# Optimization experiments

Hardware: AMD Instinct MI355X
Metric: run time of the kernel (lower is better)

Reference implementation:

```python
import jax, jax.numpy as jnp
import numpy as np

NUM_HEAD = 32
NUM_KV_HEAD = 8
HEAD_DIM = 128
EMBED_DIM = 4096
GROUP = NUM_HEAD // NUM_KV_HEAD + 2  # 6: 4 q slots + 1 k + 1 v
TOKENS = 64


def setup_inputs() -> dict:
    key = jax.random.key(0)
    k1, k2, k3 = jax.random.split(key, 3)
    inp = jax.random.normal(k1, (TOKENS, EMBED_DIM), dtype=jnp.float32)
    # fused GQA weight layout from load_parameter: [embed_dim, num_kv_head, group, head_dim]
    weight = jax.random.normal(k2, (EMBED_DIM, NUM_KV_HEAD, GROUP, HEAD_DIM), dtype=jnp.float32) * 0.02
    bias = jax.random.normal(k3, (NUM_KV_HEAD, GROUP, HEAD_DIM), dtype=jnp.float32) * 0.02
    return {"input": inp, "weight": weight, "bias": bias}


def reference(input, weight, bias):
    # fused grouped QKV GEMM (mm_qkv_group_out):
    # out[t, kv, g, d] = sum_e input[t, e] * weight[e, kv, g, d] + bias[kv, g, d]
    out = jnp.einsum('te,ekgd->tkgd', input, weight) + bias
    T = input.shape[0]
    q = out[:, :, : GROUP - 2, :].reshape(T, NUM_HEAD * HEAD_DIM)
    k = out[:, :, GROUP - 2, :].reshape(T, NUM_KV_HEAD * HEAD_DIM)
    v = out[:, :, GROUP - 1, :].reshape(T, NUM_KV_HEAD * HEAD_DIM)
    return (q, k, v)
```

## Files before the change

kernel.cpp:

```cpp
#include <hip/hip_runtime.h>


#define N_COLS 6144
#define K_DIM  4096
#define Q_SZ   (64 * 4096)
#define K_OFF  Q_SZ
#define V_OFF  (Q_SZ + 64 * 1024)
#define OUT_ELEMS 393216
#define IN_ELEMS  262144

typedef __bf16 bf16x8 __attribute__((ext_vector_type(8)));
typedef float  f32x4  __attribute__((ext_vector_type(4)));
typedef unsigned short us8 __attribute__((ext_vector_type(8)));

__device__ unsigned short g_abuf[IN_ELEMS];

__device__ __forceinline__ unsigned short f2bf_rne(float f) {
    unsigned int u = __float_as_uint(f);
    u += 0x7FFFu + ((u >> 16) & 1u);
    return (unsigned short)(u >> 16);
}

__device__ __forceinline__ int out_index(int t, int n) {
    const int kv = n / 768;
    const int g  = (n >> 7) % 6;
    const int d  = n & 127;
    if (g < 4)  return t * 4096 + kv * 512 + g * 128 + d;
    if (g == 4) return K_OFF + t * 1024 + kv * 128 + d;
    return V_OFF + t * 1024 + kv * 128 + d;
}

__global__ __launch_bounds__(256)
void init_kernel(const float* __restrict__ in, const float* __restrict__ bias,
                 float* __restrict__ out) {
    const int i = blockIdx.x * 256 + threadIdx.x;
    if (i < IN_ELEMS) g_abuf[i] = f2bf_rne(in[i]);
    if (i < OUT_ELEMS) {
        const int d   = i & 127;
        const int g   = (i >> 7) % 6;
        const int kvt = i / 768;
        const int kv  = kvt & 7;
        const int t   = kvt >> 3;
        out[out_index(t, kv * 768 + g * 128 + d)] = bias[(kv * 6 + g) * 128 + d];
    }
}

__global__ __launch_bounds__(256, 3)
void qkv_gemm(const float* __restrict__ w, float* __restrict__ out) {
    __shared__ float red[4][64][17];

    const int tid  = threadIdx.x;
    const int nt   = blockIdx.x >> 1;
    const int kh   = blockIdx.x & 1;
    const int n0   = nt * 16;
    const int wid  = tid >> 6;
    const int lane = tid & 63;
    const int l15  = lane & 15;
    const int kblk = lane >> 4;
    const int ks   = kh * 2048 + wid * 512;

    f32x4 acc[4] = {{0.f,0.f,0.f,0.f},{0.f,0.f,0.f,0.f},
                    {0.f,0.f,0.f,0.f},{0.f,0.f,0.f,0.f}};

    const float* bbase = w + (size_t)(ks + kblk * 8) * N_COLS + n0 + l15;
    const unsigned short* abase = g_abuf + l15 * K_DIM + ks + kblk * 8;

    #pragma unroll 4
    for (int kk = 0; kk < 512; kk += 32) {
        const float* bp = bbase + (size_t)kk * N_COLS;
        unsigned int b[8];
        #pragma unroll
        for (int j = 0; j < 8; ++j)
            b[j] = __float_as_uint(bp[(size_t)j * N_COLS]);

        us8 au0 = *(const us8*)(abase + kk);
        us8 au1 = *(const us8*)(abase + 16 * K_DIM + kk);
        us8 au2 = *(const us8*)(abase + 32 * K_DIM + kk);
        us8 au3 = *(const us8*)(abase + 48 * K_DIM + kk);

        union { unsigned int u[4]; us8 v; } pk;
        #pragma unroll
        for (int j = 0; j < 4; ++j) {
            const unsigned int lo = b[2 * j]     + 0x8000u;
            const unsigned int hi = b[2 * j + 1] + 0x8000u;
            pk.u[j] = (hi & 0xFFFF0000u) | (lo >> 16);
        }
        const bf16x8 bf = __builtin_bit_cast(bf16x8, pk.v);

        acc[0] = __builtin_amdgcn_mfma_f32_16x16x32_bf16(
                     __builtin_bit_cast(bf16x8, au0), bf, acc[0], 0, 0, 0);
        acc[1] = __builtin_amdgcn_mfma_f32_16x16x32_bf16(
                     __builtin_bit_cast(bf16x8, au1), bf, acc[1], 0, 0, 0);
        acc[2] = __builtin_amdgcn_mfma_f32_16x16x32_bf16(
                     __builtin_bit_cast(bf16x8, au2), bf, acc[2], 0, 0, 0);
        acc[3] = __builtin_amdgcn_mfma_f32_16x16x32_bf16(
                     __builtin_bit_cast(bf16x8, au3), bf, acc[3], 0, 0, 0);
    }

    #pragma unroll
    for (int tc = 0; tc < 4; ++tc)
        #pragma unroll
        for (int r = 0; r < 4; ++r)
            red[wid][lane][tc * 4 + r] = acc[tc][r];
    __syncthreads();

    const int l  = tid & 63;
    const int i0 = (tid >> 6) * 4;
    const int rl15  = l & 15;
    const int rkblk = l >> 4;
    #pragma unroll
    for (int r2 = 0; r2 < 4; ++r2) {
        const int i = i0 + r2;
        const float s = red[0][l][i] + red[1][l][i] + red[2][l][i] + red[3][l][i];
        const int tc = i >> 2, r = i & 3;
        const int t = tc * 16 + rkblk * 4 + r;
        atomicAdd(&out[out_index(t, n0 + rl15)], s);
    }
}

extern "C" void kernel_launch(void* const* d_in, const int* in_sizes, int n_in,
                              void* d_out, int out_size, void* d_ws, size_t ws_size,
                              hipStream_t stream) {
    const float* in   = (const float*)d_in[0];
    const float* w    = (const float*)d_in[1];
    const float* bias = (const float*)d_in[2];
    float* out = (float*)d_out;

    init_kernel<<<(OUT_ELEMS + 255) / 256, 256, 0, stream>>>(in, bias, out);
    qkv_gemm<<<768, 256, 0, stream>>>(w, out);
}
```

Before: 187.8 us.

## Split K four ways and software-pipeline weight loads with register double buffering

Raises the K split from two to four so the grid launches twice as many blocks, each warp covering 256 K elements instead of 512. The inner loop is fully unrolled and register double-buffered, prefetching the next slice of weights and activations before issuing MFMAs on the current one. Launch bounds ask for five blocks per CU to increase occupancy. The aim is more memory-level parallelism while streaming the 100MB fp32 weight, at the cost of twice as many atomic adds into the output.

Result: no change. 189.6 us (+0.9%).

```diff
diff --git a/kernel.cpp b/kernel.cpp
--- a/kernel.cpp
+++ b/kernel.cpp
@@ -8,10 +8,14 @@
 #define V_OFF  (Q_SZ + 64 * 1024)
 #define OUT_ELEMS 393216
 #define IN_ELEMS  262144
+#define KSPLIT 4
+#define KW     256
+#define NIT    (KW / 32)
 
 typedef __bf16 bf16x8 __attribute__((ext_vector_type(8)));
 typedef float  f32x4  __attribute__((ext_vector_type(4)));
 typedef unsigned short us8 __attribute__((ext_vector_type(8)));
+typedef unsigned int   u32x4 __attribute__((ext_vector_type(4)));
 
 __device__ unsigned short g_abuf[IN_ELEMS];
 
@@ -45,19 +49,30 @@
     }
 }
 
-__global__ __launch_bounds__(256, 3)
+__device__ __forceinline__ bf16x8 pack_bf16(const float* b) {
+    u32x4 pk;
+    #pragma unroll
+    for (int j = 0; j < 4; ++j) {
+        const unsigned int lo = __float_as_uint(b[2 * j])     + 0x8000u;
+        const unsigned int hi = __float_as_uint(b[2 * j + 1]) + 0x8000u;
+        pk[j] = (hi & 0xFFFF0000u) | (lo >> 16);
+    }
+    return __builtin_bit_cast(bf16x8, pk);
+}
+
+__global__ __launch_bounds__(256, 5)
 void qkv_gemm(const float* __restrict__ w, float* __restrict__ out) {
     __shared__ float red[4][64][17];
 
     const int tid  = threadIdx.x;
-    const int nt   = blockIdx.x >> 1;
-    const int kh   = blockIdx.x & 1;
+    const int nt   = blockIdx.x >> 2;
+    const int kq   = blockIdx.x & 3;
     const int n0   = nt * 16;
     const int wid  = tid >> 6;
     const int lane = tid & 63;
     const int l15  = lane & 15;
     const int kblk = lane >> 4;
-    const int ks   = kh * 2048 + wid * 512;
+    const int ks   = kq * 1024 + wid * KW;
 
     f32x4 acc[4] = {{0.f,0.f,0.f,0.f},{0.f,0.f,0.f,0.f},
                     {0.f,0.f,0.f,0.f},{0.f,0.f,0.f,0.f}};
@@ -65,36 +80,42 @@
     const float* bbase = w + (size_t)(ks + kblk * 8) * N_COLS + n0 + l15;
     const unsigned short* abase = g_abuf + l15 * K_DIM + ks + kblk * 8;
 
-    #pragma unroll 4
-    for (int kk = 0; kk < 512; kk += 32) {
-        const float* bp = bbase + (size_t)kk * N_COLS;
-        unsigned int b[8];
-        #pragma unroll
-        for (int j = 0; j < 8; ++j)
-            b[j] = __float_as_uint(bp[(size_t)j * N_COLS]);
+    float bc[8];
+    us8   ac[4];
+    #pragma unroll
+    for (int j = 0; j < 8; ++j) bc[j] = bbase[(size_t)j * N_COLS];
+    #pragma unroll
+    for (int t = 0; t < 4; ++t) ac[t] = *(const us8*)(abase + t * 16 * K_DIM);
 
-        us8 au0 = *(const us8*)(abase + kk);
-        us8 au1 = *(const us8*)(abase + 16 * K_DIM + kk);
-        us8 au2 = *(const us8*)(abase + 32 * K_DIM + kk);
-        us8 au3 = *(const us8*)(abase + 48 * K_DIM + kk);
+    #pragma unroll
+    for (int it = 0; it < NIT; ++it) {
+        float bn[8];
+        us8   an[4];
+        if (it + 1 < NIT) {
+            const float* bp = bbase + (size_t)(32 * (it + 1)) * N_COLS;
+            #pragma unroll
+            for (int j = 0; j < 8; ++j) bn[j] = bp[(size_t)j * N_COLS];
+            const unsigned short* ap = abase + 32 * (it + 1);
+            #pragma unroll
+            for (int t = 0; t < 4; ++t) an[t] = *(const us8*)(ap + t * 16 * K_DIM);
+        }
 
-        union { unsigned int u[4]; us8 v; } pk;
-        #pragma unroll
-        for (int j = 0; j < 4; ++j) {
-            const unsigned int lo = b[2 * j]     + 0x8000u;
-            const unsigned int hi = b[2 * j + 1] + 0x8000u;
-            pk.u[j] = (hi & 0xFFFF0000u) | (lo >> 16);
+        const bf16x8 bf = pack_bf16(bc);
+        acc[0] = __builtin_amdgcn_mfma_f32_16x16x32_bf16(
+                     __builtin_bit_cast(bf16x8, ac[0]), bf, acc[0], 0, 0, 0);
+        acc[1] = __builtin_amdgcn_mfma_f32_16x16x32_bf16(
+                     __builtin_bit_cast(bf16x8, ac[1]), bf, acc[1], 0, 0, 0);
+        acc[2] = __builtin_amdgcn_mfma_f32_16x16x32_bf16(
+                     __builtin_bit_cast(bf16x8, ac[2]), bf, acc[2], 0, 0, 0);
+        acc[3] = __builtin_amdgcn_mfma_f32_16x16x32_bf16(
+                     __builtin_bit_cast(bf16x8, ac[3]), bf, acc[3], 0, 0, 0);
+
+        if (it + 1 < NIT) {
+            #pragma unroll
+            for (int j = 0; j < 8; ++j) bc[j] = bn[j];
+            #pragma unroll
+            for (int t = 0; t < 4; ++t) ac[t] = an[t];
         }
-        const bf16x8 bf = __builtin_bit_cast(bf16x8, pk.v);
-
-        acc[0] = __builtin_amdgcn_mfma_f32_16x16x32_bf16(
-                     __builtin_bit_cast(bf16x8, au0), bf, acc[0], 0, 0, 0);
-        acc[1] = __builtin_amdgcn_mfma_f32_16x16x32_bf16(
-                     __builtin_bit_cast(bf16x8, au1), bf, acc[1], 0, 0, 0);
-        acc[2] = __builtin_amdgcn_mfma_f32_16x16x32_bf16(
-                     __builtin_bit_cast(bf16x8, au2), bf, acc[2], 0, 0, 0);
-        acc[3] = __builtin_amdgcn_mfma_f32_16x16x32_bf16(
-                     __builtin_bit_cast(bf16x8, au3), bf, acc[3], 0, 0, 0);
     }
 
     #pragma unroll
@@ -127,5 +148,5 @@
     float* out = (float*)d_out;
 
     init_kernel<<<(OUT_ELEMS + 255) / 256, 256, 0, stream>>>(in, bias, out);
-    qkv_gemm<<<768, 256, 0, stream>>>(w, out);
+    qkv_gemm<<<384 * KSPLIT, 256, 0, stream>>>(w, out);
 }
```

## Double-buffer global loads in QKV GEMM with inline asm and explicit vmcnt waits

Applied to the files above, without the earlier changes.

Replaces the compiler-scheduled K loop with a hand-written two-stage software pipeline. Weight and activation loads are issued through inline-asm global_load instructions into two register sets, and partial s_waitcnt vmcnt waits let one stage's MFMAs overlap the next stage's loads. Launch bounds are raised to 4 blocks per SIMD. The aim is to hide the latency of the memory-bound fp32 weight stream, at the cost of more live registers and fragile asm that assumes vmcnt ordering.

Result: no change. 186.5 us (-0.7%).

```diff
diff --git a/kernel.cpp b/kernel.cpp
--- a/kernel.cpp
+++ b/kernel.cpp
@@ -8,10 +8,13 @@
 #define V_OFF  (Q_SZ + 64 * 1024)
 #define OUT_ELEMS 393216
 #define IN_ELEMS  262144
+#define KSPLIT 2
+#define KW     512
+#define NIT    (KW / 32)
 
 typedef __bf16 bf16x8 __attribute__((ext_vector_type(8)));
 typedef float  f32x4  __attribute__((ext_vector_type(4)));
-typedef unsigned short us8 __attribute__((ext_vector_type(8)));
+typedef unsigned int u32x4 __attribute__((ext_vector_type(4)));
 
 __device__ unsigned short g_abuf[IN_ELEMS];
 
@@ -45,7 +48,56 @@
     }
 }
 
-__global__ __launch_bounds__(256, 3)
+__device__ __forceinline__ bf16x8 pack8(float f0, float f1, float f2, float f3,
+                                        float f4, float f5, float f6, float f7) {
+    u32x4 pk;
+    const float fs[8] = {f0, f1, f2, f3, f4, f5, f6, f7};
+    #pragma unroll
+    for (int j = 0; j < 4; ++j) {
+        const unsigned int lo = __float_as_uint(fs[2 * j])     + 0x8000u;
+        const unsigned int hi = __float_as_uint(fs[2 * j + 1]) + 0x8000u;
+        pk[j] = (hi & 0xFFFF0000u) | (lo >> 16);
+    }
+    return __builtin_bit_cast(bf16x8, pk);
+}
+
+#define ISSUE(P, kk) do {                                                     \
+    const float* _bp = bbase + (size_t)(kk) * N_COLS;                         \
+    asm volatile("global_load_dword %0, %1, off" : "=v"(P##_b0) : "v"(_bp + 0 * (size_t)N_COLS)); \
+    asm volatile("global_load_dword %0, %1, off" : "=v"(P##_b1) : "v"(_bp + 1 * (size_t)N_COLS)); \
+    asm volatile("global_load_dword %0, %1, off" : "=v"(P##_b2) : "v"(_bp + 2 * (size_t)N_COLS)); \
+    asm volatile("global_load_dword %0, %1, off" : "=v"(P##_b3) : "v"(_bp + 3 * (size_t)N_COLS)); \
+    asm volatile("global_load_dword %0, %1, off" : "=v"(P##_b4) : "v"(_bp + 4 * (size_t)N_COLS)); \
+    asm volatile("global_load_dword %0, %1, off" : "=v"(P##_b5) : "v"(_bp + 5 * (size_t)N_COLS)); \
+    asm volatile("global_load_dword %0, %1, off" : "=v"(P##_b6) : "v"(_bp + 6 * (size_t)N_COLS)); \
+    asm volatile("global_load_dword %0, %1, off" : "=v"(P##_b7) : "v"(_bp + 7 * (size_t)N_COLS)); \
+    const unsigned short* _ap = abase + (kk);                                 \
+    asm volatile("global_load_dwordx4 %0, %1, off" : "=v"(P##_a0) : "v"(_ap + 0 * 16 * K_DIM));   \
+    asm volatile("global_load_dwordx4 %0, %1, off" : "=v"(P##_a1) : "v"(_ap + 1 * 16 * K_DIM));   \
+    asm volatile("global_load_dwordx4 %0, %1, off" : "=v"(P##_a2) : "v"(_ap + 2 * 16 * K_DIM));   \
+    asm volatile("global_load_dwordx4 %0, %1, off" : "=v"(P##_a3) : "v"(_ap + 3 * 16 * K_DIM));   \
+} while (0)
+
+#define WAITB(P, cnt) \
+    asm volatile("s_waitcnt vmcnt(" #cnt ")"                                  \
+                 : "+v"(P##_b0), "+v"(P##_b1), "+v"(P##_b2), "+v"(P##_b3),    \
+                   "+v"(P##_b4), "+v"(P##_b5), "+v"(P##_b6), "+v"(P##_b7),    \
+                   "+v"(P##_a0), "+v"(P##_a1), "+v"(P##_a2), "+v"(P##_a3))
+
+#define CONSUME(P) do {                                                       \
+    const bf16x8 _bf = pack8(P##_b0, P##_b1, P##_b2, P##_b3,                  \
+                             P##_b4, P##_b5, P##_b6, P##_b7);                 \
+    acc[0] = __builtin_amdgcn_mfma_f32_16x16x32_bf16(                         \
+                 __builtin_bit_cast(bf16x8, P##_a0), _bf, acc[0], 0, 0, 0);   \
+    acc[1] = __builtin_amdgcn_mfma_f32_16x16x32_bf16(                         \
+                 __builtin_bit_cast(bf16x8, P##_a1), _bf, acc[1], 0, 0, 0);   \
+    acc[2] = __builtin_amdgcn_mfma_f32_16x16x32_bf16(                         \
+                 __builtin_bit_cast(bf16x8, P##_a2), _bf, acc[2], 0, 0, 0);   \
+    acc[3] = __builtin_amdgcn_mfma_f32_16x16x32_bf16(                         \
+                 __builtin_bit_cast(bf16x8, P##_a3), _bf, acc[3], 0, 0, 0);   \
+} while (0)
+
+__global__ __launch_bounds__(256, 4)
 void qkv_gemm(const float* __restrict__ w, float* __restrict__ out) {
     __shared__ float red[4][64][17];
 
@@ -57,7 +109,7 @@
     const int lane = tid & 63;
     const int l15  = lane & 15;
     const int kblk = lane >> 4;
-    const int ks   = kh * 2048 + wid * 512;
+    const int ks   = kh * 2048 + wid * KW;
 
     f32x4 acc[4] = {{0.f,0.f,0.f,0.f},{0.f,0.f,0.f,0.f},
                     {0.f,0.f,0.f,0.f},{0.f,0.f,0.f,0.f}};
@@ -65,37 +117,21 @@
     const float* bbase = w + (size_t)(ks + kblk * 8) * N_COLS + n0 + l15;
     const unsigned short* abase = g_abuf + l15 * K_DIM + ks + kblk * 8;
 
-    #pragma unroll 4
-    for (int kk = 0; kk < 512; kk += 32) {
-        const float* bp = bbase + (size_t)kk * N_COLS;
-        unsigned int b[8];
-        #pragma unroll
-        for (int j = 0; j < 8; ++j)
-            b[j] = __float_as_uint(bp[(size_t)j * N_COLS]);
+    float X_b0 = 0, X_b1 = 0, X_b2 = 0, X_b3 = 0, X_b4 = 0, X_b5 = 0, X_b6 = 0, X_b7 = 0;
+    float Y_b0 = 0, Y_b1 = 0, Y_b2 = 0, Y_b3 = 0, Y_b4 = 0, Y_b5 = 0, Y_b6 = 0, Y_b7 = 0;
+    u32x4 X_a0 = {}, X_a1 = {}, X_a2 = {}, X_a3 = {};
+    u32x4 Y_a0 = {}, Y_a1 = {}, Y_a2 = {}, Y_a3 = {};
 
-        us8 au0 = *(const us8*)(abase + kk);
-        us8 au1 = *(const us8*)(abase + 16 * K_DIM + kk);
-        us8 au2 = *(const us8*)(abase + 32 * K_DIM + kk);
-        us8 au3 = *(const us8*)(abase + 48 * K_DIM + kk);
-
-        union { unsigned int u[4]; us8 v; } pk;
-        #pragma unroll
-        for (int j = 0; j < 4; ++j) {
-            const unsigned int lo = b[2 * j]     + 0x8000u;
-            const unsigned int hi = b[2 * j + 1] + 0x8000u;
-            pk.u[j] = (hi & 0xFFFF0000u) | (lo >> 16);
-        }
-        const bf16x8 bf = __builtin_bit_cast(bf16x8, pk.v);
-
-        acc[0] = __builtin_amdgcn_mfma_f32_16x16x32_bf16(
-                     __builtin_bit_cast(bf16x8, au0), bf, acc[0], 0, 0, 0);
-        acc[1] = __builtin_amdgcn_mfma_f32_16x16x32_bf16(
-                     __builtin_bit_cast(bf16x8, au1), bf, acc[1], 0, 0, 0);
-        acc[2] = __builtin_amdgcn_mfma_f32_16x16x32_bf16(
-                     __builtin_bit_cast(bf16x8, au2), bf, acc[2], 0, 0, 0);
-        acc[3] = __builtin_amdgcn_mfma_f32_16x16x32_bf16(
-                     __builtin_bit_cast(bf16x8, au3), bf, acc[3], 0, 0, 0);
+    ISSUE(X, 0);
+    int kk = 0;
+    #pragma unroll 1
+    for (int j = 0; j < NIT / 2 - 1; ++j) {
+        ISSUE(Y, kk + 32); WAITB(X, 12); CONSUME(X);
+        ISSUE(X, kk + 64); WAITB(Y, 12); CONSUME(Y);
+        kk += 64;
     }
+    ISSUE(Y, kk + 32); WAITB(X, 12); CONSUME(X);
+    WAITB(Y, 0);       CONSUME(Y);
 
     #pragma unroll
     for (int tc = 0; tc < 4; ++tc)
@@ -127,5 +163,5 @@
     float* out = (float*)d_out;
 
     init_kernel<<<(OUT_ELEMS + 255) / 256, 256, 0, stream>>>(in, bias, out);
-    qkv_gemm<<<768, 256, 0, stream>>>(w, out);
+    qkv_gemm<<<384 * KSPLIT, 256, 0, stream>>>(w, out);
 }
```

## Stage bf16-converted weight tiles in LDS with coalesced float4 loads and 32-way split-K

Applied to the files above, without the earlier changes.

Each block now covers 256 output columns and a 128-deep K slice (32-way split-K, 768 blocks). The weight is read with coalesced float4 loads, converted to bf16 and written to shared memory, then each wave runs MFMAs over 16 column fragments for its own 16-token rows. The next K step is register-prefetched while the current one computes. The goal is to replace strided 4-byte weight gathers with wide coalesced reads, at the cost of many more global atomics (32 partials per output) and two barriers per step.

Measured after the change: 182.7 us. -2.7%, faster.

```diff
diff --git a/kernel.cpp b/kernel.cpp
--- a/kernel.cpp
+++ b/kernel.cpp
@@ -8,10 +8,13 @@
 #define V_OFF  (Q_SZ + 64 * 1024)
 #define OUT_ELEMS 393216
 #define IN_ELEMS  262144
+#define NTILES 24
+#define KSPLIT 32
+#define KSTEPS 4
 
 typedef __bf16 bf16x8 __attribute__((ext_vector_type(8)));
 typedef float  f32x4  __attribute__((ext_vector_type(4)));
-typedef unsigned short us8 __attribute__((ext_vector_type(8)));
+typedef unsigned int u32x4 __attribute__((ext_vector_type(4)));
 
 __device__ unsigned short g_abuf[IN_ELEMS];
 
@@ -45,76 +48,103 @@
     }
 }
 
+__device__ __forceinline__ unsigned int pack_pair(float lo, float hi) {
+    return ((unsigned int)f2bf_rne(hi) << 16) | f2bf_rne(lo);
+}
+
 __global__ __launch_bounds__(256, 3)
 void qkv_gemm(const float* __restrict__ w, float* __restrict__ out) {
-    __shared__ float red[4][64][17];
+    __shared__ u32x4 Bs[64][17];
 
     const int tid  = threadIdx.x;
-    const int nt   = blockIdx.x >> 1;
-    const int kh   = blockIdx.x & 1;
-    const int n0   = nt * 16;
+    const int nt   = blockIdx.x % NTILES;
+    const int kq   = blockIdx.x / NTILES;
+    const int n0   = nt * 256;
+    const int k0   = kq * (KSTEPS * 32);
+
     const int wid  = tid >> 6;
     const int lane = tid & 63;
     const int l15  = lane & 15;
     const int kblk = lane >> 4;
-    const int ks   = kh * 2048 + wid * 512;
 
-    f32x4 acc[4] = {{0.f,0.f,0.f,0.f},{0.f,0.f,0.f,0.f},
-                    {0.f,0.f,0.f,0.f},{0.f,0.f,0.f,0.f}};
+    f32x4 acc[16];
+    #pragma unroll
+    for (int i = 0; i < 16; ++i) acc[i] = (f32x4){0.f, 0.f, 0.f, 0.f};
 
-    const float* bbase = w + (size_t)(ks + kblk * 8) * N_COLS + n0 + l15;
-    const unsigned short* abase = g_abuf + l15 * K_DIM + ks + kblk * 8;
+    const float* wbase = w + (size_t)(k0 + 2 * wid) * N_COLS + n0 + 4 * lane;
+    const unsigned short* abase = g_abuf + (wid * 16 + l15) * K_DIM + k0 + kblk * 8;
 
-    #pragma unroll 4
-    for (int kk = 0; kk < 512; kk += 32) {
-        const float* bp = bbase + (size_t)kk * N_COLS;
-        unsigned int b[8];
+    float4 Lc[8], Ln[8];
+    u32x4  Ac, An;
+
+    #pragma unroll
+    for (int r = 0; r < 4; ++r) {
+        Lc[2 * r]     = *(const float4*)(wbase + (size_t)(r * 8) * N_COLS);
+        Lc[2 * r + 1] = *(const float4*)(wbase + (size_t)(r * 8 + 1) * N_COLS);
+    }
+    Ac = *(const u32x4*)abase;
+
+    const unsigned int* bsr = (const unsigned int*)&Bs[0][0];
+    const int q = l15 >> 2, ii = l15 & 3;
+
+    #pragma unroll
+    for (int s = 0; s < KSTEPS; ++s) {
         #pragma unroll
-        for (int j = 0; j < 8; ++j)
-            b[j] = __float_as_uint(bp[(size_t)j * N_COLS]);
+        for (int r = 0; r < 4; ++r) {
+            const float4 ra = Lc[2 * r], rb = Lc[2 * r + 1];
+            u32x4 cell;
+            cell[0] = pack_pair(ra.x, rb.x);
+            cell[1] = pack_pair(ra.y, rb.y);
+            cell[2] = pack_pair(ra.z, rb.z);
+            cell[3] = pack_pair(ra.w, rb.w);
+            Bs[lane][r * 4 + wid] = cell;
+        }
+        if (s + 1 < KSTEPS) {
+            const float* wn = wbase + (size_t)((s + 1) * 32) * N_COLS;
+            #pragma unroll
+            for (int r = 0; r < 4; ++r) {
+                Ln[2 * r]     = *(const float4*)(wn + (size_t)(r * 8) * N_COLS);
+                Ln[2 * r + 1] = *(const float4*)(wn + (size_t)(r * 8 + 1) * N_COLS);
+            }
+            An = *(const u32x4*)(abase + (s + 1) * 32);
+        }
+        __syncthreads();
 
-        us8 au0 = *(const us8*)(abase + kk);
-        us8 au1 = *(const us8*)(abase + 16 * K_DIM + kk);
-        us8 au2 = *(const us8*)(abase + 32 * K_DIM + kk);
-        us8 au3 = *(const us8*)(abase + 48 * K_DIM + kk);
+        const bf16x8 af = __builtin_bit_cast(bf16x8, Ac);
+        #pragma unroll
+        for (int nf = 0; nf < 16; ++nf) {
+            const unsigned int base = (unsigned)(((nf * 4 + q) * 17 + kblk * 4) * 4 + ii);
+            u32x4 bu;
+            bu[0] = bsr[base];
+            bu[1] = bsr[base + 4];
+            bu[2] = bsr[base + 8];
+            bu[3] = bsr[base + 12];
+            acc[nf] = __builtin_amdgcn_mfma_f32_16x16x32_bf16(
+                          af, __builtin_bit_cast(bf16x8, bu), acc[nf], 0, 0, 0);
+        }
+        __syncthreads();
 
-        union { unsigned int u[4]; us8 v; } pk;
-        #pragma unroll
-        for (int j = 0; j < 4; ++j) {
-            const unsigned int lo = b[2 * j]     + 0x8000u;
-            const unsigned int hi = b[2 * j + 1] + 0x8000u;
-            pk.u[j] = (hi & 0xFFFF0000u) | (lo >> 16);
+        if (s + 1 < KSTEPS) {
+            #pragma unroll
+            for (int r = 0; r < 8; ++r) Lc[r] = Ln[r];
+            Ac = An;
         }
-        const bf16x8 bf = __builtin_bit_cast(bf16x8, pk.v);
-
-        acc[0] = __builtin_amdgcn_mfma_f32_16x16x32_bf16(
-                     __builtin_bit_cast(bf16x8, au0), bf, acc[0], 0, 0, 0);
-        acc[1] = __builtin_amdgcn_mfma_f32_16x16x32_bf16(
-                     __builtin_bit_cast(bf16x8, au1), bf, acc[1], 0, 0, 0);
-        acc[2] = __builtin_amdgcn_mfma_f32_16x16x32_bf16(
-                     __builtin_bit_cast(bf16x8, au2), bf, acc[2], 0, 0, 0);
-        acc[3] = __builtin_amdgcn_mfma_f32_16x16x32_bf16(
-                     __builtin_bit_cast(bf16x8, au3), bf, acc[3], 0, 0, 0);
     }
 
     #pragma unroll
-    for (int tc = 0; tc < 4; ++tc)
+    for (int nf = 0; nf < 16; ++nf) {
+        const int nb = n0 + nf * 16;
+        const int kv = nb / 768;
+        const int g  = (nb >> 7) % 6;
+        const int d  = (nb & 127) + l15;
+        int base, tstride;
+        if (g < 4)       { base = kv * 512 + g * 128 + d;  tstride = 4096; }
+        else if (g == 4) { base = K_OFF + kv * 128 + d;    tstride = 1024; }
+        else             { base = V_OFF + kv * 128 + d;    tstride = 1024; }
+        const int t0 = wid * 16 + kblk * 4;
         #pragma unroll
         for (int r = 0; r < 4; ++r)
-            red[wid][lane][tc * 4 + r] = acc[tc][r];
-    __syncthreads();
-
-    const int l  = tid & 63;
-    const int i0 = (tid >> 6) * 4;
-    const int rl15  = l & 15;
-    const int rkblk = l >> 4;
-    #pragma unroll
-    for (int r2 = 0; r2 < 4; ++r2) {
-        const int i = i0 + r2;
-        const float s = red[0][l][i] + red[1][l][i] + red[2][l][i] + red[3][l][i];
-        const int tc = i >> 2, r = i & 3;
-        const int t = tc * 16 + rkblk * 4 + r;
-        atomicAdd(&out[out_index(t, n0 + rl15)], s);
+            atomicAdd(&out[base + (t0 + r) * tstride], acc[nf][r]);
     }
 }
 
@@ -127,5 +157,5 @@
     float* out = (float*)d_out;
 
     init_kernel<<<(OUT_ELEMS + 255) / 256, 256, 0, stream>>>(in, bias, out);
-    qkv_gemm<<<768, 256, 0, stream>>>(w, out);
+    qkv_gemm<<<NTILES * KSPLIT, 256, 0, stream>>>(w, out);
 }
```
